# Kernel tuning notes

Hardware: AMD Instinct MI355X
Metric: run time of the kernel (lower is better)

## Reference

```python
import jax, jax.numpy as jnp
import numpy as np

B, S, D, H = 2, 2048, 1024, 16
HD = D // H  # head_dim = 64


def setup_inputs() -> dict:
    key = jax.random.key(0)
    k1, k2, k3, k4, k5 = jax.random.split(key, 5)
    x = jax.random.normal(k1, (B, S, D), dtype=jnp.float32)
    # causal additive mask [S, S]: 0 on/below diagonal, -1e9 above
    mask = jnp.where(jnp.tril(jnp.ones((S, S), dtype=bool)), 0.0, -1e9).astype(jnp.float32)
    scale = 1.0 / np.sqrt(D)
    W_qkv = jax.random.normal(k2, (D, 3 * D), dtype=jnp.float32) * scale
    b_qkv = jax.random.normal(k3, (3 * D,), dtype=jnp.float32) * 0.01
    W_o = jax.random.normal(k4, (D, D), dtype=jnp.float32) * scale
    b_o = jax.random.normal(k5, (D,), dtype=jnp.float32) * 0.01
    return {"x": x, "mask": mask, "W_qkv": W_qkv, "b_qkv": b_qkv, "W_o": W_o, "b_o": b_o}


def reference(x, mask, W_qkv, b_qkv, W_o, b_o):
    b, s, d = x.shape
    qkv = x @ W_qkv + b_qkv                         # [B,S,3D]
    qkv = qkv.reshape(b, s, H, 3 * HD).transpose(0, 2, 1, 3)  # [B,H,S,3*HD]
    q, k, v = jnp.split(qkv, 3, axis=-1)            # each [B,H,S,HD]
    scores = jnp.einsum('bhqd,bhkd->bhqk', q, k) / np.sqrt(HD)  # [B,H,S,S]
    scores = scores + mask                           # broadcast [S,S] additive mask
    attn = jax.nn.softmax(scores, axis=-1)
    vals = jnp.einsum('bhqk,bhkd->bhqd', attn, v)    # [B,H,S,HD]
    vals = vals.transpose(0, 2, 1, 3).reshape(b, s, d)
    return vals @ W_o + b_o
```

## Files before the change

kernel.cpp:

```cpp
#include <hip/hip_runtime.h>

#define NB 2
#define NS 2048
#define ND 1024
#define NH 16
#define NHD 64
#define QLD (3 * ND)
#define PADP 72
#define PADV 68

typedef unsigned short u16;
typedef __attribute__((ext_vector_type(8))) short short8;
typedef __attribute__((ext_vector_type(4))) short short4v;
typedef __attribute__((ext_vector_type(4))) float f32x4;

__device__ __forceinline__ u16 f2b(float f) {
    unsigned int x = __float_as_uint(f);
    return (u16)((x + 0x7fffu + ((x >> 16) & 1u)) >> 16);
}

__global__ __launch_bounds__(256) void convert_bf16(
    const float* __restrict__ src, u16* __restrict__ dst, int n)
{
    const int i = (blockIdx.x * 256 + threadIdx.x) * 8;
    if (i >= n) return;
    float4 a = *(const float4*)(src + i);
    float4 b = *(const float4*)(src + i + 4);
    *(ushort4*)(dst + i)     = make_ushort4(f2b(a.x), f2b(a.y), f2b(a.z), f2b(a.w));
    *(ushort4*)(dst + i + 4) = make_ushort4(f2b(b.x), f2b(b.y), f2b(b.z), f2b(b.w));
}

__global__ __launch_bounds__(256) void transpose_bf16(
    const float* __restrict__ W, u16* __restrict__ WT, int K, int N)
{
    __shared__ u16 Ts[64 * 72];
    const int t = threadIdx.x;
    const int k0 = blockIdx.y << 6, n0 = blockIdx.x << 6;
    const int r = t >> 4, c = (t & 15) << 2;
    #pragma unroll
    for (int rr = 0; rr < 64; rr += 16) {
        float4 v = *(const float4*)&W[(size_t)(k0 + r + rr) * N + n0 + c];
        Ts[(c + 0) * 72 + r + rr] = f2b(v.x);
        Ts[(c + 1) * 72 + r + rr] = f2b(v.y);
        Ts[(c + 2) * 72 + r + rr] = f2b(v.z);
        Ts[(c + 3) * 72 + r + rr] = f2b(v.w);
    }
    __syncthreads();
    const int n = t >> 2, cc = (t & 3) << 4;
    uint4 a = *(const uint4*)&Ts[n * 72 + cc];
    uint4 b = *(const uint4*)&Ts[n * 72 + cc + 8];
    *(uint4*)&WT[(size_t)(n0 + n) * K + k0 + cc]     = a;
    *(uint4*)&WT[(size_t)(n0 + n) * K + k0 + cc + 8] = b;
}

template <bool STORE_BF16>
__global__ __launch_bounds__(256) void gemm_mfma(
    const u16* __restrict__ A, const u16* __restrict__ BT,
    const float* __restrict__ bias,
    void* __restrict__ C, int M, int N, int K)
{
    __shared__ u16 As[128 * 32];
    __shared__ u16 Bs[128 * 32];

    const int tid = threadIdx.x;
    const int wave = tid >> 6, lane = tid & 63;
    const int col = lane & 15, quad = lane >> 4;
    const int wm = wave >> 1, wn = wave & 1;
    const int row0 = blockIdx.y << 7, col0 = blockIdx.x << 7;

    f32x4 acc[4][4] = {};

    const u16* asrc[2];
    const u16* bsrc[2];
    u16* adst[2];
    u16* bdst[2];
    #pragma unroll
    for (int is = 0; is < 2; ++is) {
        const int J = is * 256 + wave * 64 + lane;
        const int m = J >> 2;
        const int q = (J & 3) ^ ((m >> 1) & 3);
        asrc[is] = A  + (size_t)(row0 + m) * K + q * 8;
        bsrc[is] = BT + (size_t)(col0 + m) * K + q * 8;
        adst[is] = &As[(size_t)(is * 256 + wave * 64) * 8];
        bdst[is] = &Bs[(size_t)(is * 256 + wave * 64) * 8];
    }

    for (int kk = 0; kk < K; kk += 32) {
        __syncthreads();
        #pragma unroll
        for (int is = 0; is < 2; ++is) {
            __builtin_amdgcn_global_load_lds(
                (const __attribute__((address_space(1))) unsigned int*)(asrc[is] + kk),
                (__attribute__((address_space(3))) unsigned int*)adst[is], 16, 0, 0);
            __builtin_amdgcn_global_load_lds(
                (const __attribute__((address_space(1))) unsigned int*)(bsrc[is] + kk),
                (__attribute__((address_space(3))) unsigned int*)bdst[is], 16, 0, 0);
        }
        __syncthreads();

        short8 af[4], bf[4];
        #pragma unroll
        for (int i = 0; i < 4; ++i) {
            const int m = wm * 64 + i * 16 + col;
            af[i] = *(const short8*)&As[(m * 4 + (quad ^ ((m >> 1) & 3))) * 8];
        }
        #pragma unroll
        for (int j = 0; j < 4; ++j) {
            const int n = wn * 64 + j * 16 + col;
            bf[j] = *(const short8*)&Bs[(n * 4 + (quad ^ ((n >> 1) & 3))) * 8];
        }
        #pragma unroll
        for (int i = 0; i < 4; ++i)
            #pragma unroll
            for (int j = 0; j < 4; ++j)
                acc[i][j] = __builtin_amdgcn_mfma_f32_16x16x32_bf16(
                    af[i], bf[j], acc[i][j], 0, 0, 0);
    }

    #pragma unroll
    for (int j = 0; j < 4; ++j) {
        const int gc = col0 + wn * 64 + j * 16 + col;
        const float bj = bias[gc];
        #pragma unroll
        for (int i = 0; i < 4; ++i) {
            const int gr = row0 + wm * 64 + i * 16 + quad * 4;
            #pragma unroll
            for (int r = 0; r < 4; ++r) {
                const float v = acc[i][j][r] + bj;
                if (STORE_BF16)
                    ((u16*)C)[(size_t)(gr + r) * N + gc] = f2b(v);
                else
                    ((float*)C)[(size_t)(gr + r) * N + gc] = v;
            }
        }
    }
}

__global__ __launch_bounds__(256) void attn_kernel(
    const u16* __restrict__ qkv, u16* __restrict__ vals)
{
    __shared__ u16 Ks[2][64 * 64];
    __shared__ u16 Vt[2][64 * PADV];
    __shared__ u16 Ps[64 * PADP];

    const int tid = threadIdx.x;
    const int wave = tid >> 6, lane = tid & 63;
    const int col = lane & 15, quad = lane >> 4;
    const int qtA = blockIdx.x;
    const int qtB = 31 - qtA;
    const int bh = blockIdx.y;
    const int b = bh >> 4, h = bh & 15;
    const size_t base = (size_t)b * NS * QLD + (size_t)h * (3 * NHD);
    const int q0 = wave * 16;
    const int qloc = q0 + col;

    int Jrow[2], Jcol[2];
    #pragma unroll
    for (int is = 0; is < 2; ++is) {
        const int J = is * 256 + wave * 64 + lane;
        Jrow[is] = J >> 3;
        Jcol[is] = ((J & 7) ^ (Jrow[is] & 7)) << 3;
    }

    auto stage_tile = [&](int buf, int srow, int coloff) {
        #pragma unroll
        for (int is = 0; is < 2; ++is) {
            __builtin_amdgcn_global_load_lds(
                (const __attribute__((address_space(1))) unsigned int*)
                    (qkv + base + (size_t)(srow + Jrow[is]) * QLD + coloff + Jcol[is]),
                (__attribute__((address_space(3))) unsigned int*)
                    &Ks[buf][(size_t)(is * 256 + wave * 64) * 8], 16, 0, 0);
        }
    };
    auto read_frag = [&](int buf, int row, int half) -> short8 {
        const int blk = row * 8 + ((quad + (half << 2)) ^ (row & 7));
        return *(const short8*)&Ks[buf][blk << 3];
    };

    const int vtx = tid & 15, vty = tid >> 4;
    const int vk0 = vty << 2, vd0 = vtx << 2;
    auto load_vregs = [&](int kt, ushort4* vr) {
        const u16* vsrc = qkv + base + (size_t)(kt * 64 + vk0) * QLD + 2 * NHD + vd0;
        vr[0] = *(const ushort4*)(vsrc);
        vr[1] = *(const ushort4*)(vsrc + QLD);
        vr[2] = *(const ushort4*)(vsrc + 2 * QLD);
        vr[3] = *(const ushort4*)(vsrc + 3 * QLD);
    };
    auto write_vt = [&](int buf, const ushort4* vr) {
        *(ushort4*)&Vt[buf][(vd0 + 0) * PADV + vk0] =
            make_ushort4(vr[0].x, vr[1].x, vr[2].x, vr[3].x);
        *(ushort4*)&Vt[buf][(vd0 + 1) * PADV + vk0] =
            make_ushort4(vr[0].y, vr[1].y, vr[2].y, vr[3].y);
        *(ushort4*)&Vt[buf][(vd0 + 2) * PADV + vk0] =
            make_ushort4(vr[0].z, vr[1].z, vr[2].z, vr[3].z);
        *(ushort4*)&Vt[buf][(vd0 + 3) * PADV + vk0] =
            make_ushort4(vr[0].w, vr[1].w, vr[2].w, vr[3].w);
    };

    stage_tile(0, qtA * 64, 0);
    stage_tile(1, qtB * 64, 0);
    __syncthreads();
    short8 bqA0 = read_frag(0, qloc, 0), bqA1 = read_frag(0, qloc, 1);
    short8 bqB0 = read_frag(1, qloc, 0), bqB1 = read_frag(1, qloc, 1);
    __syncthreads();

    f32x4 accA[4] = {}, accB[4] = {};
    float mA = -1e30f, lA = 0.f, mB = -1e30f, lB = 0.f;

    auto process = [&](const short8& b0, const short8& b1,
                       short8 (*kb)[2], short8 (*vb)[2],
                       f32x4* accO, float& m, float& l, bool diag) {
        f32x4 s[4] = {};
        #pragma unroll
        for (int kg = 0; kg < 4; ++kg) {
            s[kg] = __builtin_amdgcn_mfma_f32_16x16x32_bf16(kb[kg][0], b0, s[kg], 0, 0, 0);
            s[kg] = __builtin_amdgcn_mfma_f32_16x16x32_bf16(kb[kg][1], b1, s[kg], 0, 0, 0);
        }
        #pragma unroll
        for (int kg = 0; kg < 4; ++kg)
            #pragma unroll
            for (int r = 0; r < 4; ++r) {
                float v = s[kg][r] * 0.125f;
                if (diag && (kg * 16 + quad * 4 + r > qloc)) v = -1e30f;
                s[kg][r] = v;
            }
        float mx = -1e30f;
        #pragma unroll
        for (int kg = 0; kg < 4; ++kg)
            mx = fmaxf(mx, fmaxf(fmaxf(s[kg][0], s[kg][1]), fmaxf(s[kg][2], s[kg][3])));
        mx = fmaxf(mx, __shfl_xor(mx, 16, 64));
        mx = fmaxf(mx, __shfl_xor(mx, 32, 64));
        const float mn = fmaxf(m, mx);
        const float alpha = __expf(m - mn);
        m = mn;

        float ps = 0.f;
        #pragma unroll
        for (int kg = 0; kg < 4; ++kg) {
            float p0 = __expf(s[kg][0] - mn);
            float p1 = __expf(s[kg][1] - mn);
            float p2 = __expf(s[kg][2] - mn);
            float p3 = __expf(s[kg][3] - mn);
            ps += (p0 + p1) + (p2 + p3);
            *(ushort4*)&Ps[qloc * PADP + kg * 16 + quad * 4] =
                make_ushort4(f2b(p0), f2b(p1), f2b(p2), f2b(p3));
        }
        ps += __shfl_xor(ps, 16, 64);
        ps += __shfl_xor(ps, 32, 64);
        l = l * alpha + ps;
        #pragma unroll
        for (int dg = 0; dg < 4; ++dg)
            #pragma unroll
            for (int r = 0; r < 4; ++r) accO[dg][r] *= alpha;

        short8 pb0 = *(const short8*)&Ps[qloc * PADP + quad * 8];
        short8 pb1 = *(const short8*)&Ps[qloc * PADP + 32 + quad * 8];
        #pragma unroll
        for (int dg = 0; dg < 4; ++dg) {
            accO[dg] = __builtin_amdgcn_mfma_f32_16x16x32_bf16(vb[dg][0], pb0, accO[dg], 0, 0, 0);
            accO[dg] = __builtin_amdgcn_mfma_f32_16x16x32_bf16(vb[dg][1], pb1, accO[dg], 0, 0, 0);
        }
    };

    ushort4 vcur[4], vnxt[4];
    stage_tile(0, 0, NHD);
    load_vregs(0, vcur);

    for (int kt = 0; kt <= qtB; ++kt) {
        const int cur = kt & 1, nxt = cur ^ 1;
        __syncthreads();
        write_vt(cur, vcur);
        __syncthreads();
        if (kt < qtB) {
            stage_tile(nxt, (kt + 1) * 64, NHD);
            load_vregs(kt + 1, vnxt);
        }

        short8 kb[4][2], vb[4][2];
        #pragma unroll
        for (int kg = 0; kg < 4; ++kg) {
            kb[kg][0] = read_frag(cur, kg * 16 + col, 0);
            kb[kg][1] = read_frag(cur, kg * 16 + col, 1);
        }
        #pragma unroll
        for (int dg = 0; dg < 4; ++dg) {
            const int n = dg * 16 + col;
            short4v lo0 = *(const short4v*)&Vt[cur][n * PADV + quad * 8];
            short4v hi0 = *(const short4v*)&Vt[cur][n * PADV + quad * 8 + 4];
            short4v lo1 = *(const short4v*)&Vt[cur][n * PADV + 32 + quad * 8];
            short4v hi1 = *(const short4v*)&Vt[cur][n * PADV + 32 + quad * 8 + 4];
            vb[dg][0] = __builtin_shufflevector(lo0, hi0, 0, 1, 2, 3, 4, 5, 6, 7);
            vb[dg][1] = __builtin_shufflevector(lo1, hi1, 0, 1, 2, 3, 4, 5, 6, 7);
        }

        process(bqB0, bqB1, kb, vb, accB, mB, lB, kt == qtB);
        if (kt <= qtA)
            process(bqA0, bqA1, kb, vb, accA, mA, lA, kt == qtA);

        #pragma unroll
        for (int i = 0; i < 4; ++i) vcur[i] = vnxt[i];
    }

    {
        const float inv = 1.f / lA;
        const size_t rowoff = ((size_t)b * NS + qtA * 64 + qloc) * ND + h * NHD;
        #pragma unroll
        for (int dg = 0; dg < 4; ++dg) {
            ushort4 o;
            o.x = f2b(accA[dg][0] * inv);
            o.y = f2b(accA[dg][1] * inv);
            o.z = f2b(accA[dg][2] * inv);
            o.w = f2b(accA[dg][3] * inv);
            *(ushort4*)(vals + rowoff + dg * 16 + quad * 4) = o;
        }
    }
    {
        const float inv = 1.f / lB;
        const size_t rowoff = ((size_t)b * NS + qtB * 64 + qloc) * ND + h * NHD;
        #pragma unroll
        for (int dg = 0; dg < 4; ++dg) {
            ushort4 o;
            o.x = f2b(accB[dg][0] * inv);
            o.y = f2b(accB[dg][1] * inv);
            o.z = f2b(accB[dg][2] * inv);
            o.w = f2b(accB[dg][3] * inv);
            *(ushort4*)(vals + rowoff + dg * 16 + quad * 4) = o;
        }
    }
}

extern "C" void kernel_launch(void* const* d_in, const int* in_sizes, int n_in,
                              void* d_out, int out_size, void* d_ws, size_t ws_size,
                              hipStream_t stream)
{
    const float* x    = (const float*)d_in[0];
    const float* Wqkv = (const float*)d_in[2];
    const float* bqkv = (const float*)d_in[3];
    const float* Wo   = (const float*)d_in[4];
    const float* bo   = (const float*)d_in[5];
    float* out = (float*)d_out;

    u16* x_bf   = (u16*)d_ws;
    u16* WqkvT  = x_bf   + (size_t)4096 * 1024;
    u16* WoT    = WqkvT  + (size_t)3072 * 1024;
    u16* qkv    = WoT    + (size_t)1024 * 1024;
    u16* vals   = qkv    + (size_t)4096 * 3072;

    const int M = NB * NS;

    convert_bf16<<<dim3(M * ND / (256 * 8)), dim3(256), 0, stream>>>(
        x, x_bf, M * ND);
    transpose_bf16<<<dim3(QLD / 64, ND / 64), dim3(256), 0, stream>>>(
        Wqkv, WqkvT, ND, QLD);
    transpose_bf16<<<dim3(ND / 64, ND / 64), dim3(256), 0, stream>>>(
        Wo, WoT, ND, ND);

    gemm_mfma<true><<<dim3(QLD / 128, M / 128), dim3(256), 0, stream>>>(
        x_bf, WqkvT, bqkv, qkv, M, QLD, ND);
    attn_kernel<<<dim3(16, NB * NH), dim3(256), 0, stream>>>(qkv, vals);
    gemm_mfma<false><<<dim3(ND / 128, M / 128), dim3(256), 0, stream>>>(
        vals, WoT, bo, out, M, ND, ND);
}
```

Baseline: 219.9 us.

## Double-buffer GEMM LDS tiles and vectorize epilogue via swapped MFMA operands

```diff
diff --git a/kernel.cpp b/kernel.cpp
--- a/kernel.cpp
+++ b/kernel.cpp
@@ -59,8 +59,8 @@
     const float* __restrict__ bias,
     void* __restrict__ C, int M, int N, int K)
 {
-    __shared__ u16 As[128 * 32];
-    __shared__ u16 Bs[128 * 32];
+    __shared__ u16 As[2][128 * 32];
+    __shared__ u16 Bs[2][128 * 32];
 
     const int tid = threadIdx.x;
     const int wave = tid >> 6, lane = tid & 63;
@@ -72,8 +72,7 @@
 
     const u16* asrc[2];
     const u16* bsrc[2];
-    u16* adst[2];
-    u16* bdst[2];
+    int dstoff[2];
     #pragma unroll
     for (int is = 0; is < 2; ++is) {
         const int J = is * 256 + wave * 64 + lane;
@@ -81,56 +80,66 @@
         const int q = (J & 3) ^ ((m >> 1) & 3);
         asrc[is] = A  + (size_t)(row0 + m) * K + q * 8;
         bsrc[is] = BT + (size_t)(col0 + m) * K + q * 8;
-        adst[is] = &As[(size_t)(is * 256 + wave * 64) * 8];
-        bdst[is] = &Bs[(size_t)(is * 256 + wave * 64) * 8];
-    }
-
-    for (int kk = 0; kk < K; kk += 32) {
-        __syncthreads();
+        dstoff[is] = (is * 256 + wave * 64) * 8;
+    }
+
+    auto stage = [&](int buf, int kk) {
         #pragma unroll
         for (int is = 0; is < 2; ++is) {
             __builtin_amdgcn_global_load_lds(
                 (const __attribute__((address_space(1))) unsigned int*)(asrc[is] + kk),
-                (__attribute__((address_space(3))) unsigned int*)adst[is], 16, 0, 0);
+                (__attribute__((address_space(3))) unsigned int*)&As[buf][dstoff[is]],
+                16, 0, 0);
             __builtin_amdgcn_global_load_lds(
                 (const __attribute__((address_space(1))) unsigned int*)(bsrc[is] + kk),
-                (__attribute__((address_space(3))) unsigned int*)bdst[is], 16, 0, 0);
-        }
+                (__attribute__((address_space(3))) unsigned int*)&Bs[buf][dstoff[is]],
+                16, 0, 0);
+        }
+    };
+
+    stage(0, 0);
+    int ib = 0;
+    for (int kk = 0; kk < K; kk += 32, ib ^= 1) {
         __syncthreads();
+        if (kk + 32 < K)
+            stage(ib ^ 1, kk + 32);
 
         short8 af[4], bf[4];
         #pragma unroll
         for (int i = 0; i < 4; ++i) {
             const int m = wm * 64 + i * 16 + col;
-            af[i] = *(const short8*)&As[(m * 4 + (quad ^ ((m >> 1) & 3))) * 8];
+            af[i] = *(const short8*)&As[ib][(m * 4 + (quad ^ ((m >> 1) & 3))) * 8];
         }
         #pragma unroll
         for (int j = 0; j < 4; ++j) {
             const int n = wn * 64 + j * 16 + col;
-            bf[j] = *(const short8*)&Bs[(n * 4 + (quad ^ ((n >> 1) & 3))) * 8];
+            bf[j] = *(const short8*)&Bs[ib][(n * 4 + (quad ^ ((n >> 1) & 3))) * 8];
         }
         #pragma unroll
         for (int i = 0; i < 4; ++i)
             #pragma unroll
             for (int j = 0; j < 4; ++j)
                 acc[i][j] = __builtin_amdgcn_mfma_f32_16x16x32_bf16(
-                    af[i], bf[j], acc[i][j], 0, 0, 0);
+                    bf[j], af[i], acc[i][j], 0, 0, 0);
     }
 
     #pragma unroll
-    for (int j = 0; j < 4; ++j) {
-        const int gc = col0 + wn * 64 + j * 16 + col;
-        const float bj = bias[gc];
-        #pragma unroll
-        for (int i = 0; i < 4; ++i) {
-            const int gr = row0 + wm * 64 + i * 16 + quad * 4;
-            #pragma unroll
-            for (int r = 0; r < 4; ++r) {
-                const float v = acc[i][j][r] + bj;
-                if (STORE_BF16)
-                    ((u16*)C)[(size_t)(gr + r) * N + gc] = f2b(v);
-                else
-                    ((float*)C)[(size_t)(gr + r) * N + gc] = v;
+    for (int i = 0; i < 4; ++i) {
+        const int gm = row0 + wm * 64 + i * 16 + col;
+        #pragma unroll
+        for (int j = 0; j < 4; ++j) {
+            const int gn = col0 + wn * 64 + j * 16 + quad * 4;
+            float4 bj = *(const float4*)(bias + gn);
+            float v0 = acc[i][j][0] + bj.x;
+            float v1 = acc[i][j][1] + bj.y;
+            float v2 = acc[i][j][2] + bj.z;
+            float v3 = acc[i][j][3] + bj.w;
+            if (STORE_BF16) {
+                *(ushort4*)((u16*)C + (size_t)gm * N + gn) =
+                    make_ushort4(f2b(v0), f2b(v1), f2b(v2), f2b(v3));
+            } else {
+                *(float4*)((float*)C + (size_t)gm * N + gn) =
+                    make_float4(v0, v1, v2, v3);
             }
         }
     }
```

Measured after the change: 233.1 us. 1.06x slower.
